# Kernel tuning notes

Hardware: AMD Instinct MI355X
Metric: run time of the kernel (lower is better)

## Reference

```python
import jax, jax.numpy as jnp
import numpy as np
import math

D_MODEL = 1024
NUM_HEAD = 16
D_HEAD = D_MODEL // NUM_HEAD
SEQ = 2048
BATCH = 2


def setup_inputs() -> dict:
    key = jax.random.key(0)
    k1, k2, k3, k4, k5 = jax.random.split(key, 5)
    s = 1.0 / math.sqrt(D_MODEL)
    return {
        "x": jax.random.normal(k1, (SEQ, BATCH, D_MODEL), dtype=jnp.float32),
        "qkv_w": jax.random.normal(k2, (3 * D_MODEL, D_MODEL), dtype=jnp.float32) * s,
        "qkv_b": jax.random.normal(k3, (3 * D_MODEL,), dtype=jnp.float32) * 0.01,
        "out_w": jax.random.normal(k4, (D_MODEL, D_MODEL), dtype=jnp.float32) * s,
        "out_b": jax.random.normal(k5, (D_MODEL,), dtype=jnp.float32) * 0.01,
        "is_causal": 1,
    }


def reference(x, qkv_w, qkv_b, out_w, out_b, is_causal):
    t, b, _ = x.shape
    qkv = x @ qkv_w.T + qkv_b  # [t, b, 3*d_model]
    # 't b (k h d) -> b k h t d'
    qkv = qkv.reshape(t, b, 3, NUM_HEAD, D_HEAD).transpose(1, 2, 3, 0, 4)
    q, k, v = qkv[:, 0], qkv[:, 1], qkv[:, 2]  # each [b, h, t, d]
    softmax_scale = 1.0 / math.sqrt(D_HEAD)
    # NOTE: faithful to source bug: score is DIVIDED by softmax_scale
    score = jnp.einsum('bhtd,bhsd->bhts', q, k) / softmax_scale
    if is_causal:
        causal_mask = jnp.triu(jnp.full((t, t), -1000000.0, dtype=score.dtype), k=1)
        score = score + causal_mask
    attn = jax.nn.softmax(score, axis=-1)
    av = jnp.einsum('bhts,bhsd->bhtd', attn, v)  # [b, h, t, d]
    av = av.transpose(2, 0, 1, 3).reshape(t, b, D_MODEL)  # 'b h t d -> t b (h d)'
    return av @ out_w.T + out_b
```

## Files before the change

### kernel.cpp

```cpp
#include <hip/hip_runtime.h>
#include <math.h>

#define TSEQ   2048
#define BB     2
#define DMODEL 1024
#define NHEAD  16
#define DHEAD  64
#define MROWS  (TSEQ * BB)

typedef __attribute__((ext_vector_type(8))) _Float16 half8;
typedef __attribute__((ext_vector_type(4))) float    floatx4;
typedef unsigned short u16;
typedef unsigned int   u32;

#define QSCL 11.5415603f
#define MSK  1442695.0f

__device__ __forceinline__ u16 f2h(float f) {
    union { _Float16 h; u16 u; } cv;
    cv.h = (_Float16)f;
    return cv.u;
}

__device__ __forceinline__ u32 pkrtz(float a, float b) {
    typedef __attribute__((ext_vector_type(2))) __fp16 fp16x2;
    union { fp16x2 h; u32 u; } cv;
    cv.h = __builtin_amdgcn_cvt_pkrtz(a, b);
    return cv.u;
}

__device__ __forceinline__ void async_cp16(const u16* g, u16* l) {
    __builtin_amdgcn_global_load_lds(
        (const __attribute__((address_space(1))) unsigned int*)g,
        (__attribute__((address_space(3))) unsigned int*)l, 16, 0, 0);
}

__global__ __launch_bounds__(256)
void cast3_f32_f16(const float* __restrict__ a, u16* __restrict__ oa,
                   const float* __restrict__ b, u16* __restrict__ ob,
                   const float* __restrict__ c, u16* __restrict__ oc)
{
    int i = blockIdx.x * 256 + threadIdx.x;
    const float* src; u16* dst; int off;
    if (i < 1048576)      { src = a; dst = oa; off = 0; }
    else if (i < 1835008) { src = b; dst = ob; off = 1048576; }
    else                  { src = c; dst = oc; off = 1835008; }
    int j = i - off;
    float4 v = ((const float4*)src)[j];
    ushort4 o;
    o.x = f2h(v.x); o.y = f2h(v.y); o.z = f2h(v.z); o.w = f2h(v.w);
    ((ushort4*)dst)[j] = o;
}

__global__ __launch_bounds__(512)
void gemm_qkv(const u16* __restrict__ A, const u16* __restrict__ W,
              const float* __restrict__ bias,
              u16* __restrict__ Qo, u16* __restrict__ Ko, u16* __restrict__ Vo,
              int M, int N, int K)
{
    __shared__ __align__(16) u16 As[128][64];
    __shared__ __align__(16) u16 Bs[128][64];

    const int tid  = threadIdx.x;
    const int lane = tid & 63;
    const int wv   = tid >> 6;
    const int wr   = wv >> 1;
    const int wc   = wv & 1;
    const int ln   = lane & 15, lh = lane >> 4;
    const int m0   = blockIdx.y * 128;
    const int n0   = blockIdx.x * 128;

    const int c = n0 >> 10;
    const bool vmode = (c == 2);

    const floatx4 zero4 = {0.0f, 0.0f, 0.0f, 0.0f};
    floatx4 acc[2][4];
#pragma unroll
    for (int i = 0; i < 2; ++i)
#pragma unroll
        for (int j = 0; j < 4; ++j) acc[i][j] = zero4;

    for (int k0 = 0; k0 < K; k0 += 64) {
        __syncthreads();
#pragma unroll
        for (int t = 0; t < 2; ++t) {
            const int u    = t * 512 + tid;
            const int row  = u >> 3;
            const int slot = u & 7;
            const int g    = slot ^ (row & 7);
            async_cp16(A + (size_t)(m0 + row) * K + k0 + g * 8, &As[row][slot * 8]);
            async_cp16(W + (size_t)(n0 + row) * K + k0 + g * 8, &Bs[row][slot * 8]);
        }
        __syncthreads();

#pragma unroll
        for (int ks = 0; ks < 2; ++ks) {
            half8 xf[2], wf[4];
#pragma unroll
            for (int i = 0; i < 2; ++i) {
                const int row = wr * 32 + i * 16 + ln;
                xf[i] = *(const half8*)&As[row][(((ks << 2) | lh) ^ (row & 7)) * 8];
            }
#pragma unroll
            for (int j = 0; j < 4; ++j) {
                const int row = wc * 64 + j * 16 + ln;
                wf[j] = *(const half8*)&Bs[row][(((ks << 2) | lh) ^ (row & 7)) * 8];
            }
            if (vmode) {
#pragma unroll
                for (int i = 0; i < 2; ++i)
#pragma unroll
                    for (int j = 0; j < 4; ++j)
                        acc[i][j] = __builtin_amdgcn_mfma_f32_16x16x32_f16(xf[i], wf[j], acc[i][j], 0, 0, 0);
            } else {
#pragma unroll
                for (int i = 0; i < 2; ++i)
#pragma unroll
                    for (int j = 0; j < 4; ++j)
                        acc[i][j] = __builtin_amdgcn_mfma_f32_16x16x32_f16(wf[j], xf[i], acc[i][j], 0, 0, 0);
            }
        }
    }

    if (!vmode) {
        const float scl = (c == 0) ? QSCL : 1.0f;
        u16* dst = (c == 0) ? Qo : Ko;
#pragma unroll
        for (int j = 0; j < 4; ++j) {
            const int nb = n0 + wc * 64 + j * 16 + lh * 4;
            const float4 b4 = *(const float4*)&bias[nb];
            const int h  = (nb >> 6) & 15;
            const int d0 = nb & 63;
#pragma unroll
            for (int i = 0; i < 2; ++i) {
                const int tok = m0 + wr * 32 + i * 16 + ln;
                const int t = tok >> 1, b = tok & 1;
                uint2 pk;
                pk.x = pkrtz((acc[i][j][0] + b4.x) * scl, (acc[i][j][1] + b4.y) * scl);
                pk.y = pkrtz((acc[i][j][2] + b4.z) * scl, (acc[i][j][3] + b4.w) * scl);
                *(uint2*)&dst[(((size_t)b * NHEAD + h) * TSEQ + t) * DHEAD + d0] = pk;
            }
        }
    } else {
#pragma unroll
        for (int j = 0; j < 4; ++j) {
            const int col = n0 + wc * 64 + j * 16 + ln;
            const float bc = bias[col];
            const int h = (col >> 6) & 15;
            const int d = col & 63;
#pragma unroll
            for (int i = 0; i < 2; ++i) {
                const int mb = m0 + wr * 32 + i * 16 + lh * 4;
                const int t0 = mb >> 1;
                const u32 e0 = pkrtz(acc[i][j][0] + bc, acc[i][j][2] + bc);
                const u32 e1 = pkrtz(acc[i][j][1] + bc, acc[i][j][3] + bc);
                *(u32*)&Vo[(((size_t)0 * NHEAD + h) * DHEAD + d) * TSEQ + t0] = e0;
                *(u32*)&Vo[(((size_t)1 * NHEAD + h) * DHEAD + d) * TSEQ + t0] = e1;
            }
        }
    }
}

__global__ __launch_bounds__(256)
void gemm_out64(const u16* __restrict__ A, const u16* __restrict__ W,
                const float* __restrict__ bias, float* __restrict__ Cout,
                int M, int N, int K)
{
    __shared__ __align__(16) u16 As[64][128];
    __shared__ __align__(16) u16 Bs[64][128];

    const int tid  = threadIdx.x;
    const int lane = tid & 63;
    const int wv   = tid >> 6;
    const int ln   = lane & 15, lh = lane >> 4;

    const int bidlin = blockIdx.y * 16 + blockIdx.x;
    const int wg  = (bidlin & 7) * 128 + (bidlin >> 3);
    const int bx  = wg & 15, by = wg >> 4;
    const int m0  = by * 64;
    const int n0  = bx * 64;

    const floatx4 zero4 = {0.0f, 0.0f, 0.0f, 0.0f};
    floatx4 acc[4];
#pragma unroll
    for (int j = 0; j < 4; ++j) acc[j] = zero4;

    for (int k0 = 0; k0 < K; k0 += 128) {
        __syncthreads();
#pragma unroll
        for (int u = 0; u < 4; ++u) {
            const int idx  = u * 256 + tid;
            const int row  = idx >> 4;
            const int slot = idx & 15;
            const int g    = (slot & 8) | ((slot & 7) ^ (row & 7));
            async_cp16(A + (size_t)(m0 + row) * K + k0 + g * 8, &As[row][slot * 8]);
            async_cp16(W + (size_t)(n0 + row) * K + k0 + g * 8, &Bs[row][slot * 8]);
        }
        __syncthreads();

#pragma unroll
        for (int ks = 0; ks < 4; ++ks) {
            const int arow = wv * 16 + ln;
            half8 xf = *(const half8*)&As[arow][(((ks << 2) | lh) ^ (arow & 7)) * 8];
#pragma unroll
            for (int j = 0; j < 4; ++j) {
                const int row = j * 16 + ln;
                half8 wf = *(const half8*)&Bs[row][(((ks << 2) | lh) ^ (row & 7)) * 8];
                acc[j] = __builtin_amdgcn_mfma_f32_16x16x32_f16(wf, xf, acc[j], 0, 0, 0);
            }
        }
    }

#pragma unroll
    for (int j = 0; j < 4; ++j) {
        const int fb = n0 + j * 16 + lh * 4;
        const float4 b4 = *(const float4*)&bias[fb];
        const int tok = m0 + wv * 16 + ln;
        float4 v;
        v.x = acc[j][0] + b4.x;
        v.y = acc[j][1] + b4.y;
        v.z = acc[j][2] + b4.z;
        v.w = acc[j][3] + b4.w;
        *(float4*)&Cout[(size_t)tok * N + fb] = v;
    }
}

__global__ __launch_bounds__(256, 4)
void flash_f16(const u16* __restrict__ Q, const u16* __restrict__ K,
               const u16* __restrict__ Vt, u16* __restrict__ AV,
               const int* __restrict__ causal_p)
{
    __shared__ __align__(16) u16 smem[192 * 64];
    u16 (* __restrict__ Ps)[64] = (u16(*)[64])smem;
    u16 (* __restrict__ Ks)[64] = (u16(*)[64])(smem + 64 * 64);
    u16 (* __restrict__ Vs)[64] = (u16(*)[64])(smem + 128 * 64);

    const int tid  = threadIdx.x;
    const int lane = tid & 63;
    const int wv   = tid >> 6;
    const int ln   = lane & 15, lh = lane >> 4;

    const int phase = blockIdx.x >> 8;
    const int slot  = blockIdx.x & 255;
    const int bh    = slot & 31;
    const int jq    = slot >> 5;
    int qb;
    if      (phase == 0) qb = 31 - jq;
    else if (phase == 1) qb = jq;
    else if (phase == 2) qb = 23 - jq;
    else                 qb = 8 + jq;

    const int b = bh >> 4;
    const int h = bh & 15;
    const int causal = causal_p[0];

    const u16* Qg = Q  + (size_t)bh * TSEQ * DHEAD;
    const u16* Kg = K  + (size_t)bh * TSEQ * DHEAD;
    const u16* Vg = Vt + (size_t)bh * DHEAD * TSEQ;

    const int lrow = tid >> 3;
    const int lc8  = (tid & 7) * 8;
    const int lg8  = ((tid & 7) ^ (lrow & 7)) * 8;

    const int qr0   = wv * 16;
    const int qloc  = qr0 + ln;
    const int s7    = ln & 7;
    const int qglob = qb * 64 + qloc;

    const half8 bQ0 = *(const half8*)(Qg + (size_t)qglob * DHEAD + lh * 8);
    const half8 bQ1 = *(const half8*)(Qg + (size_t)qglob * DHEAD + 32 + lh * 8);

    const _Float16 ov = (_Float16)((ln == 0) ? 1.0f : 0.0f);
    const half8 ones = {ov, ov, ov, ov, ov, ov, ov, ov};

    const floatx4 zero4 = {0.0f, 0.0f, 0.0f, 0.0f};
    floatx4 o[4], o4;
#pragma unroll
    for (int j = 0; j < 4; ++j) o[j] = zero4;
    o4 = zero4;
    float m_i = -3.0e38f;

    const int kb_end = causal ? qb : (TSEQ / 64 - 1);

    uint4 kreg0 = *(const uint4*)(Kg + (size_t)lrow * DHEAD + lc8);
    uint4 kreg1 = *(const uint4*)(Kg + (size_t)(lrow + 32) * DHEAD + lc8);
    uint4 vreg0 = *(const uint4*)(Vg + (size_t)lrow * TSEQ + lc8);
    uint4 vreg1 = *(const uint4*)(Vg + (size_t)(lrow + 32) * TSEQ + lc8);

    for (int kb = 0; kb <= kb_end; ++kb) {
        *(uint4*)&Ks[lrow][lg8]      = kreg0;
        *(uint4*)&Ks[lrow + 32][lg8] = kreg1;
        *(uint4*)&Vs[lrow][lg8]      = vreg0;
        *(uint4*)&Vs[lrow + 32][lg8] = vreg1;
        __syncthreads();

        if (kb < kb_end) {
            const size_t nk = (size_t)(kb + 1) * 64;
            kreg0 = *(const uint4*)(Kg + (nk + lrow) * DHEAD + lc8);
            kreg1 = *(const uint4*)(Kg + (nk + lrow + 32) * DHEAD + lc8);
            vreg0 = *(const uint4*)(Vg + (size_t)lrow * TSEQ + nk + lc8);
            vreg1 = *(const uint4*)(Vg + (size_t)(lrow + 32) * TSEQ + nk + lc8);
        }

        floatx4 s[4];
        __builtin_amdgcn_s_setprio(1);
#pragma unroll
        for (int j = 0; j < 4; ++j) {
            half8 aK0 = *(const half8*)&Ks[j * 16 + ln][(lh ^ s7) * 8];
            half8 aK1 = *(const half8*)&Ks[j * 16 + ln][((4 | lh) ^ s7) * 8];
            floatx4 z = zero4;
            z = __builtin_amdgcn_mfma_f32_16x16x32_f16(aK0, bQ0, z, 0, 0, 0);
            z = __builtin_amdgcn_mfma_f32_16x16x32_f16(aK1, bQ1, z, 0, 0, 0);
            s[j] = z;
        }
        __builtin_amdgcn_s_setprio(0);

        half8 bV[8];
#pragma unroll
        for (int j = 0; j < 4; ++j) {
            bV[2 * j]     = *(const half8*)&Vs[j * 16 + ln][(lh ^ s7) * 8];
            bV[2 * j + 1] = *(const half8*)&Vs[j * 16 + ln][((4 | lh) ^ s7) * 8];
        }

        if ((causal != 0) && (kb == qb)) {
#pragma unroll
            for (int j = 0; j < 4; ++j)
#pragma unroll
                for (int r = 0; r < 4; ++r)
                    if (j * 16 + lh * 4 + r > qloc) s[j][r] -= MSK;
        }

        float mx = m_i;
#pragma unroll
        for (int j = 0; j < 4; ++j)
#pragma unroll
            for (int r = 0; r < 4; ++r) mx = fmaxf(mx, s[j][r]);
        mx = fmaxf(mx, __shfl_xor(mx, 16));
        mx = fmaxf(mx, __shfl_xor(mx, 32));

        if (!__all(mx <= m_i + 8.0f)) {
            const float alpha = exp2f(m_i - mx);
            m_i = mx;
            float a_r[4];
#pragma unroll
            for (int r = 0; r < 4; ++r) a_r[r] = __shfl(alpha, lh * 4 + r);
#pragma unroll
            for (int j = 0; j < 4; ++j)
#pragma unroll
                for (int r = 0; r < 4; ++r) o[j][r] *= a_r[r];
#pragma unroll
            for (int r = 0; r < 4; ++r) o4[r] *= a_r[r];
        }

#pragma unroll
        for (int j = 0; j < 4; ++j) {
            uint2 pk;
            pk.x = pkrtz(exp2f(s[j][0] - m_i), exp2f(s[j][1] - m_i));
            pk.y = pkrtz(exp2f(s[j][2] - m_i), exp2f(s[j][3] - m_i));
            *(uint2*)&Ps[qloc][(((2 * j + (lh >> 1)) ^ s7) * 8) + (lh & 1) * 4] = pk;
        }

        half8 aP0 = *(const half8*)&Ps[qloc][(lh ^ s7) * 8];
        half8 aP1 = *(const half8*)&Ps[qloc][((4 | lh) ^ s7) * 8];
        __builtin_amdgcn_s_setprio(1);
#pragma unroll
        for (int j = 0; j < 4; ++j) {
            o[j] = __builtin_amdgcn_mfma_f32_16x16x32_f16(aP0, bV[2 * j],     o[j], 0, 0, 0);
            o[j] = __builtin_amdgcn_mfma_f32_16x16x32_f16(aP1, bV[2 * j + 1], o[j], 0, 0, 0);
        }
        o4 = __builtin_amdgcn_mfma_f32_16x16x32_f16(aP0, ones, o4, 0, 0, 0);
        o4 = __builtin_amdgcn_mfma_f32_16x16x32_f16(aP1, ones, o4, 0, 0, 0);
        __builtin_amdgcn_s_setprio(0);

        __syncthreads();
    }

#pragma unroll
    for (int r = 0; r < 4; ++r) {
        const float lr = __shfl(o4[r], lane & 48);
        const float il = 1.0f / lr;
        const int qrow = qb * 64 + qr0 + lh * 4 + r;
#pragma unroll
        for (int j = 0; j < 4; ++j) {
            const int d = j * 16 + ln;
            AV[((size_t)qrow * BB + b) * DMODEL + h * 64 + d] = f2h(o[j][r] * il);
        }
    }
}

extern "C" void kernel_launch(void* const* d_in, const int* in_sizes, int n_in,
                              void* d_out, int out_size, void* d_ws, size_t ws_size,
                              hipStream_t stream)
{
    const float* x      = (const float*)d_in[0];
    const float* qkv_w  = (const float*)d_in[1];
    const float* qkv_b  = (const float*)d_in[2];
    const float* out_w  = (const float*)d_in[3];
    const float* out_b  = (const float*)d_in[4];
    const int*   is_causal = (const int*)d_in[5];
    float* out = (float*)d_out;

    u16* ws   = (u16*)d_ws;
    u16* xb   = ws;
    u16* wqkv = xb   + (size_t)4194304;
    u16* wout = wqkv + (size_t)3145728;
    u16* Qh   = wout + (size_t)1048576;
    u16* Kh   = Qh   + (size_t)4194304;
    u16* Vth  = Kh   + (size_t)4194304;
    u16* AVh  = Vth  + (size_t)4194304;

    cast3_f32_f16<<<8192, 256, 0, stream>>>(x, xb, qkv_w, wqkv, out_w, wout);

    gemm_qkv<<<dim3(3 * DMODEL / 128, MROWS / 128), 512, 0, stream>>>(
        xb, wqkv, qkv_b, Qh, Kh, Vth, MROWS, 3 * DMODEL, DMODEL);

    flash_f16<<<1024, 256, 0, stream>>>(Qh, Kh, Vth, AVh, is_causal);

    gemm_out64<<<dim3(DMODEL / 64, MROWS / 64), 256, 0, stream>>>(
        AVh, wout, out_b, out, MROWS, DMODEL, DMODEL);
}
```

Before: 183.3 us.

## Split attention KV range across two blocks and merge partials in separate kernel

```diff
diff --git a/kernel.cpp b/kernel.cpp
--- a/kernel.cpp
+++ b/kernel.cpp
@@ -225,9 +225,11 @@
     }
 }
 
-__global__ __launch_bounds__(256, 4)
+__global__ __launch_bounds__(256, 6)
 void flash_f16(const u16* __restrict__ Q, const u16* __restrict__ K,
-               const u16* __restrict__ Vt, u16* __restrict__ AV,
+               const u16* __restrict__ Vt,
+               float* __restrict__ Ou, float* __restrict__ Mp,
+               float* __restrict__ Lp,
                const int* __restrict__ causal_p)
 {
     __shared__ __align__(16) u16 smem[192 * 64];
@@ -240,19 +242,17 @@
     const int wv   = tid >> 6;
     const int ln   = lane & 15, lh = lane >> 4;
 
-    const int phase = blockIdx.x >> 8;
-    const int slot  = blockIdx.x & 255;
-    const int bh    = slot & 31;
-    const int jq    = slot >> 5;
-    int qb;
-    if      (phase == 0) qb = 31 - jq;
-    else if (phase == 1) qb = jq;
-    else if (phase == 2) qb = 23 - jq;
-    else                 qb = 8 + jq;
-
-    const int b = bh >> 4;
-    const int h = bh & 15;
+    const int bid   = blockIdx.x;
+    const int split = bid & 1;
+    const int tile  = bid >> 1;
+    const int bh    = tile & 31;
+    const int qb    = 31 - (tile >> 5);
+
     const int causal = causal_p[0];
+    const int n    = causal ? (qb + 1) : (TSEQ / 64);
+    const int half = (n + 1) >> 1;
+    const int kb_beg = split ? half : 0;
+    const int kb_end = split ? n : half;
 
     const u16* Qg = Q  + (size_t)bh * TSEQ * DHEAD;
     const u16* Kg = K  + (size_t)bh * TSEQ * DHEAD;
@@ -280,21 +280,20 @@
     o4 = zero4;
     float m_i = -3.0e38f;
 
-    const int kb_end = causal ? qb : (TSEQ / 64 - 1);
-
-    uint4 kreg0 = *(const uint4*)(Kg + (size_t)lrow * DHEAD + lc8);
-    uint4 kreg1 = *(const uint4*)(Kg + (size_t)(lrow + 32) * DHEAD + lc8);
-    uint4 vreg0 = *(const uint4*)(Vg + (size_t)lrow * TSEQ + lc8);
-    uint4 vreg1 = *(const uint4*)(Vg + (size_t)(lrow + 32) * TSEQ + lc8);
-
-    for (int kb = 0; kb <= kb_end; ++kb) {
+    const size_t kb0 = (size_t)kb_beg * 64;
+    uint4 kreg0 = *(const uint4*)(Kg + (kb0 + lrow) * DHEAD + lc8);
+    uint4 kreg1 = *(const uint4*)(Kg + (kb0 + lrow + 32) * DHEAD + lc8);
+    uint4 vreg0 = *(const uint4*)(Vg + (size_t)lrow * TSEQ + kb0 + lc8);
+    uint4 vreg1 = *(const uint4*)(Vg + (size_t)(lrow + 32) * TSEQ + kb0 + lc8);
+
+    for (int kb = kb_beg; kb < kb_end; ++kb) {
         *(uint4*)&Ks[lrow][lg8]      = kreg0;
         *(uint4*)&Ks[lrow + 32][lg8] = kreg1;
         *(uint4*)&Vs[lrow][lg8]      = vreg0;
         *(uint4*)&Vs[lrow + 32][lg8] = vreg1;
         __syncthreads();
 
-        if (kb < kb_end) {
+        if (kb + 1 < kb_end) {
             const size_t nk = (size_t)(kb + 1) * 64;
             kreg0 = *(const uint4*)(Kg + (nk + lrow) * DHEAD + lc8);
             kreg1 = *(const uint4*)(Kg + (nk + lrow + 32) * DHEAD + lc8);
@@ -327,7 +326,7 @@
             for (int j = 0; j < 4; ++j)
 #pragma unroll
                 for (int r = 0; r < 4; ++r)
-                    if (j * 16 + lh * 4 + r > qloc) s[j][r] -= MSK;
+                    if (kb * 64 + j * 16 + lh * 4 + r - kb * 64 > qloc) s[j][r] -= MSK;
         }
 
         float mx = m_i;
@@ -375,16 +374,64 @@
         __syncthreads();
     }
 
+    float* Obase = Ou + (size_t)bid * 4096;
 #pragma unroll
     for (int r = 0; r < 4; ++r) {
         const float lr = __shfl(o4[r], lane & 48);
-        const float il = 1.0f / lr;
-        const int qrow = qb * 64 + qr0 + lh * 4 + r;
-#pragma unroll
-        for (int j = 0; j < 4; ++j) {
-            const int d = j * 16 + ln;
-            AV[((size_t)qrow * BB + b) * DMODEL + h * 64 + d] = f2h(o[j][r] * il);
-        }
+        const float il = (lr > 0.0f) ? 1.0f / lr : 0.0f;
+        const float mr = __shfl(m_i, lh * 4 + r);
+        const int row = qr0 + lh * 4 + r;
+        if (ln == 0) {
+            Mp[(size_t)bid * 64 + row] = mr;
+            Lp[(size_t)bid * 64 + row] = lr;
+        }
+#pragma unroll
+        for (int j = 0; j < 4; ++j)
+            Obase[row * 64 + j * 16 + ln] = o[j][r] * il;
+    }
+}
+
+__global__ __launch_bounds__(256)
+void flash_merge(const float* __restrict__ Ou, const float* __restrict__ Mp,
+                 const float* __restrict__ Lp, u16* __restrict__ AV)
+{
+    __shared__ float w1s[64], w2s[64];
+
+    const int tile = blockIdx.x;
+    const int bh   = tile & 31;
+    const int qb   = 31 - (tile >> 5);
+    const int b = bh >> 4, h = bh & 15;
+    const int tid = threadIdx.x;
+    const size_t t0 = (size_t)tile * 2;
+
+    if (tid < 64) {
+        const float m1 = Mp[t0 * 64 + tid], m2 = Mp[(t0 + 1) * 64 + tid];
+        const float l1 = Lp[t0 * 64 + tid], l2 = Lp[(t0 + 1) * 64 + tid];
+        const float m  = fmaxf(m1, m2);
+        const float e1 = exp2f(m1 - m), e2 = exp2f(m2 - m);
+        const float inv = 1.0f / (l1 * e1 + l2 * e2);
+        w1s[tid] = l1 * e1 * inv;
+        w2s[tid] = l2 * e2 * inv;
+    }
+    __syncthreads();
+
+    const float* O1 = Ou + t0 * 4096;
+    const float* O2 = O1 + 4096;
+#pragma unroll
+    for (int e = 0; e < 4; ++e) {
+        const int elem = e * 1024 + tid * 4;
+        const int row  = elem >> 6;
+        const int col  = elem & 63;
+        const float4 a = *(const float4*)&O1[elem];
+        const float4 c = *(const float4*)&O2[elem];
+        const float w1 = w1s[row], w2 = w2s[row];
+        ushort4 pk;
+        pk.x = f2h(a.x * w1 + c.x * w2);
+        pk.y = f2h(a.y * w1 + c.y * w2);
+        pk.z = f2h(a.z * w1 + c.z * w2);
+        pk.w = f2h(a.w * w1 + c.w * w2);
+        const int qrow = qb * 64 + row;
+        *(ushort4*)&AV[((size_t)qrow * BB + b) * DMODEL + h * 64 + col] = pk;
     }
 }
 
@@ -408,13 +455,17 @@
     u16* Kh   = Qh   + (size_t)4194304;
     u16* Vth  = Kh   + (size_t)4194304;
     u16* AVh  = Vth  + (size_t)4194304;
+    float* Oup = (float*)(AVh + (size_t)4194304);
+    float* Mpp = Oup + (size_t)8388608;
+    float* Lpp = Mpp + (size_t)131072;
 
     cast3_f32_f16<<<8192, 256, 0, stream>>>(x, xb, qkv_w, wqkv, out_w, wout);
 
     gemm_qkv<<<dim3(3 * DMODEL / 128, MROWS / 128), 512, 0, stream>>>(
         xb, wqkv, qkv_b, Qh, Kh, Vth, MROWS, 3 * DMODEL, DMODEL);
 
-    flash_f16<<<1024, 256, 0, stream>>>(Qh, Kh, Vth, AVh, is_causal);
+    flash_f16<<<2048, 256, 0, stream>>>(Qh, Kh, Vth, Oup, Mpp, Lpp, is_causal);
+    flash_merge<<<1024, 256, 0, stream>>>(Oup, Mpp, Lpp, AVh);
 
     gemm_out64<<<dim3(DMODEL / 64, MROWS / 64), 256, 0, stream>>>(
         AVh, wout, out_b, out, MROWS, DMODEL, DMODEL);
```

Result: slower. 381.3 us (+108.1%).
